# Performance work log

Hardware: AMD Instinct MI355X
Metric: run time of the kernel (lower is better)

Reference implementation:

```python
import jax, jax.numpy as jnp
import numpy as np

IN_FEATURES = 512
OUT_FEATURES = 512
BATCH = 1024


def setup_inputs() -> dict:
    key = jax.random.key(0)
    k_x, k_bw, k_ww, k_sc, k_tr, k_b = jax.random.split(key, 6)
    std = 1.0 / np.sqrt(IN_FEATURES)
    x = jax.random.normal(k_x, (BATCH, IN_FEATURES), dtype=jnp.float32)
    base_weight = jax.random.uniform(k_bw, (OUT_FEATURES, IN_FEATURES), jnp.float32, -std, std)
    wavelet_weights = jax.random.uniform(k_ww, (OUT_FEATURES, IN_FEATURES), jnp.float32, -std, std)
    # scale initialized to ones in the module; perturb slightly (kept positive) for a non-degenerate test
    scale = jnp.exp(0.1 * jax.random.normal(k_sc, (OUT_FEATURES, IN_FEATURES), dtype=jnp.float32))
    translation = 0.1 * jax.random.normal(k_tr, (OUT_FEATURES, IN_FEATURES), dtype=jnp.float32)
    bias = jax.random.uniform(k_b, (OUT_FEATURES,), jnp.float32, -std, std)
    return {"x": x, "base_weight": base_weight, "wavelet_weights": wavelet_weights,
            "scale": scale, "translation": translation, "bias": bias}


def reference(x, base_weight, wavelet_weights, scale, translation, bias):
    # base branch: SiLU then linear
    base_out = jnp.einsum("bi,oi->bo", jax.nn.silu(x), base_weight)
    # wavelet branch: broadcast x to (batch, out, in)
    xs = (x[:, None, :] - translation[None, :, :]) / scale[None, :, :]  # (B, O, I)
    wavelet = (xs * xs - 1.0) * jnp.exp(-0.5 * xs * xs)  # mexican hat
    wavelet_out = jnp.einsum("boi,oi->bo", wavelet, wavelet_weights)
    return base_out + wavelet_out + bias
```

## Files before the change

kernel.cpp:

```cpp
#include <hip/hip_runtime.h>


constexpr int IN_F  = 512;
constexpr int OUT_F = 512;
constexpr int BATCH = 1024;
constexpr int BT = 64, OT = 64;
constexpr int KS = 8;
constexpr int KR = IN_F / KS;
constexpr int IT = 16;
constexpr int PITCH = IT + 4;
constexpr int NCH = KR / IT;
constexpr int BO  = BATCH * OUT_F;

#define LOG2E 1.44269504088897f
#define C2f   (-0.72134752044448f)
#define NC2f  ( 0.72134752044448f)
#define RQf   (-0.84083003f)

typedef float v2f __attribute__((ext_vector_type(2)));

__device__ __forceinline__ float fexp2(float v) { return __builtin_amdgcn_exp2f(v); }
__device__ __forceinline__ float frcp(float v)  { return __builtin_amdgcn_rcpf(v); }
__device__ __forceinline__ v2f pkfma(v2f a, v2f b, v2f c) {
  return __builtin_elementwise_fma(a, b, c);
}
__device__ __forceinline__ float fsilu(float v) {
  return v * frcp(1.f + fexp2(v * -LOG2E));
}

__global__ __launch_bounds__(256, 4)
void wkan_main(const float* __restrict__ x, const float* __restrict__ basew,
               const float* __restrict__ wavew, const float* __restrict__ scale,
               const float* __restrict__ transl, const float* __restrict__ bias,
               float* __restrict__ partial, float* __restrict__ out, int use_ws)
{
  __shared__ float lx [BT * PITCH];
  __shared__ float lsx[BT * PITCH];
  __shared__ float la [OT * PITCH];
  __shared__ float lm [OT * PITCH];
  __shared__ float ln [OT * PITCH];
  __shared__ float lq [OT * PITCH];
  __shared__ float lb [OT * PITCH];

  const int tid = threadIdx.x;
  const int b0 = blockIdx.x * BT;
  const int o0 = blockIdx.y * OT;
  const int ks = blockIdx.z;
  const int k0 = ks * KR;

  const int srow = tid >> 2;
  const int sc4  = (tid & 3) * 4;
  const int lofs = srow * PITCH + sc4;

  const int to = tid & 15;
  const int tb = tid >> 4;

  v2f zz; zz.x = 0.f; zz.y = 0.f;
  v2f acc[4][4];
#pragma unroll
  for (int r = 0; r < 4; ++r)
#pragma unroll
    for (int c = 0; c < 4; ++c) acc[r][c] = zz;

  for (int kc = 0; kc < NCH; ++kc) {
    const int g = k0 + kc * IT + sc4;
    __syncthreads();
    {
      float4 xv = *(const float4*)(x + (size_t)(b0 + srow) * IN_F + g);
      float4 sx;
      sx.x = fsilu(xv.x); sx.y = fsilu(xv.y); sx.z = fsilu(xv.z); sx.w = fsilu(xv.w);
      *(float4*)(lx  + lofs) = xv;
      *(float4*)(lsx + lofs) = sx;

      float4 sv = *(const float4*)(scale  + (size_t)(o0 + srow) * IN_F + g);
      float4 tv = *(const float4*)(transl + (size_t)(o0 + srow) * IN_F + g);
      float4 av, mv, nv;
      {
        float a2, a2t;
        a2 = C2f * frcp(sv.x * sv.x); a2t = a2 * tv.x;
        av.x = a2; mv.x = -2.f * a2t; nv.x = fmaf(a2t, tv.x, NC2f);
        a2 = C2f * frcp(sv.y * sv.y); a2t = a2 * tv.y;
        av.y = a2; mv.y = -2.f * a2t; nv.y = fmaf(a2t, tv.y, NC2f);
        a2 = C2f * frcp(sv.z * sv.z); a2t = a2 * tv.z;
        av.z = a2; mv.z = -2.f * a2t; nv.z = fmaf(a2t, tv.z, NC2f);
        a2 = C2f * frcp(sv.w * sv.w); a2t = a2 * tv.w;
        av.w = a2; mv.w = -2.f * a2t; nv.w = fmaf(a2t, tv.w, NC2f);
      }
      *(float4*)(la + lofs) = av;
      *(float4*)(lm + lofs) = mv;
      *(float4*)(ln + lofs) = nv;

      float4 wv = *(const float4*)(wavew + (size_t)(o0 + srow) * IN_F + g);
      float4 qv;
      qv.x = wv.x * RQf; qv.y = wv.y * RQf; qv.z = wv.z * RQf; qv.w = wv.w * RQf;
      *(float4*)(lq + lofs) = qv;

      float4 bv = *(const float4*)(basew + (size_t)(o0 + srow) * IN_F + g);
      *(float4*)(lb + lofs) = bv;
    }
    __syncthreads();

    for (int ii = 0; ii < IT; ii += 4) {
      float4 xr[4], sr[4], x2[4];
#pragma unroll
      for (int r = 0; r < 4; ++r) {
        const int row = (tb + 16 * r) * PITCH + ii;
        xr[r] = *(const float4*)(lx + row);
        sr[r] = *(const float4*)(lsx + row);
        x2[r].x = xr[r].x * xr[r].x;
        x2[r].y = xr[r].y * xr[r].y;
        x2[r].z = xr[r].z * xr[r].z;
        x2[r].w = xr[r].w * xr[r].w;
      }
#pragma unroll
      for (int c = 0; c < 4; ++c) {
        const int orow = (to + 16 * c) * PITCH + ii;
        float4 A = *(const float4*)(la + orow);
        float4 M = *(const float4*)(lm + orow);
        float4 N = *(const float4*)(ln + orow);
        float4 Q = *(const float4*)(lq + orow);
        float4 B = *(const float4*)(lb + orow);
        v2f Al = {A.x, A.y}, Ah = {A.z, A.w};
        v2f Ml = {M.x, M.y}, Mh = {M.z, M.w};
        v2f Nl = {N.x, N.y}, Nh = {N.z, N.w};
        v2f Ql = {Q.x, Q.y}, Qh = {Q.z, Q.w};
        v2f Bl = {B.x, B.y}, Bh = {B.z, B.w};
#pragma unroll
        for (int r = 0; r < 4; ++r) {
          v2f xl  = {xr[r].x, xr[r].y}, xh  = {xr[r].z, xr[r].w};
          v2f x2l = {x2[r].x, x2[r].y}, x2h = {x2[r].z, x2[r].w};
          v2f sl  = {sr[r].x, sr[r].y}, sh  = {sr[r].z, sr[r].w};
          v2f p, e, gg;
          p = pkfma(Al, x2l, pkfma(Ml, xl, Nl));
          e.x = fexp2(p.x); e.y = fexp2(p.y);
          gg = p * Ql;
          acc[r][c] = pkfma(gg, e, acc[r][c]);
          acc[r][c] = pkfma(sl, Bl, acc[r][c]);
          p = pkfma(Ah, x2h, pkfma(Mh, xh, Nh));
          e.x = fexp2(p.x); e.y = fexp2(p.y);
          gg = p * Qh;
          acc[r][c] = pkfma(gg, e, acc[r][c]);
          acc[r][c] = pkfma(sh, Bh, acc[r][c]);
        }
      }
    }
  }

#pragma unroll
  for (int r = 0; r < 4; ++r) {
    const int br = b0 + tb + 16 * r;
#pragma unroll
    for (int c = 0; c < 4; ++c) {
      const int oc = o0 + to + 16 * c;
      float res = acc[r][c].x + acc[r][c].y;
      if (use_ws) {
        partial[(size_t)ks * BO + (size_t)br * OUT_F + oc] = res;
      } else {
        if (ks == 0) res += bias[oc];
        atomicAdd(out + (size_t)br * OUT_F + oc, res);
      }
    }
  }
}

__global__ __launch_bounds__(256)
void wkan_reduce(const float* __restrict__ partial, const float* __restrict__ bias,
                 float* __restrict__ out)
{
  const int i4 = (blockIdx.x * 256 + threadIdx.x) * 4;
  float4 r = *(const float4*)(bias + (i4 & (OUT_F - 1)));
#pragma unroll
  for (int k = 0; k < KS; ++k) {
    float4 a = *(const float4*)(partial + (size_t)k * BO + i4);
    r.x += a.x; r.y += a.y; r.z += a.z; r.w += a.w;
  }
  *(float4*)(out + i4) = r;
}

extern "C" void kernel_launch(void* const* d_in, const int* in_sizes, int n_in,
                              void* d_out, int out_size, void* d_ws, size_t ws_size,
                              hipStream_t stream) {
  const float* x  = (const float*)d_in[0];
  const float* bw = (const float*)d_in[1];
  const float* ww = (const float*)d_in[2];
  const float* sc = (const float*)d_in[3];
  const float* tr = (const float*)d_in[4];
  const float* bi = (const float*)d_in[5];
  float* out = (float*)d_out;

  const int use_ws = ws_size >= (size_t)KS * BO * sizeof(float) ? 1 : 0;
  if (!use_ws) {
    hipMemsetAsync(d_out, 0, (size_t)out_size * sizeof(float), stream);
  }
  dim3 grid(BATCH / BT, OUT_F / OT, KS);
  wkan_main<<<grid, dim3(256), 0, stream>>>(x, bw, ww, sc, tr, bi,
                                            (float*)d_ws, out, use_ws);
  if (use_ws) {
    wkan_reduce<<<dim3(BO / 1024), dim3(256), 0, stream>>>((const float*)d_ws, bi, out);
  }
}
```

Baseline: 115.2 us.

## Move SiLU base branch to fp16 MFMA and prefetch next chunk into registers

The SiLU-linear base branch leaves the scalar packed-FMA loop and runs as fp16 16x16x16 MFMA ops on half-precision tiles of silu(x) and base_weight. Its result goes through shared memory and is added to the wavelet accumulator at the end. The global loads for the next k-chunk are now issued before the compute of the current chunk to hide latency, and shared memory is merged into one aliased buffer. This removes VALU work from the exp-bound inner loop, but fp16 inputs lower accuracy and the extra LDS round trip adds syncs.

```diff
diff --git a/kernel.cpp b/kernel.cpp
--- a/kernel.cpp
+++ b/kernel.cpp
@@ -9,6 +9,8 @@
 constexpr int KR = IN_F / KS;
 constexpr int IT = 16;
 constexpr int PITCH = IT + 4;
+constexpr int HP = IT + 4;
+constexpr int LP = OT + 1;
 constexpr int NCH = KR / IT;
 constexpr int BO  = BATCH * OUT_F;
 
@@ -17,7 +19,9 @@
 #define NC2f  ( 0.72134752044448f)
 #define RQf   (-0.84083003f)
 
-typedef float v2f __attribute__((ext_vector_type(2)));
+typedef float v2f   __attribute__((ext_vector_type(2)));
+typedef float f32x4 __attribute__((ext_vector_type(4)));
+typedef _Float16 half4 __attribute__((ext_vector_type(4)));
 
 __device__ __forceinline__ float fexp2(float v) { return __builtin_amdgcn_exp2f(v); }
 __device__ __forceinline__ float frcp(float v)  { return __builtin_amdgcn_rcpf(v); }
@@ -27,6 +31,8 @@
 __device__ __forceinline__ float fsilu(float v) {
   return v * frcp(1.f + fexp2(v * -LOG2E));
 }
+
+constexpr int SMEM_F = 7680;
 
 __global__ __launch_bounds__(256, 4)
 void wkan_main(const float* __restrict__ x, const float* __restrict__ basew,
@@ -34,13 +40,15 @@
                const float* __restrict__ transl, const float* __restrict__ bias,
                float* __restrict__ partial, float* __restrict__ out, int use_ws)
 {
-  __shared__ float lx [BT * PITCH];
-  __shared__ float lsx[BT * PITCH];
-  __shared__ float la [OT * PITCH];
-  __shared__ float lm [OT * PITCH];
-  __shared__ float ln [OT * PITCH];
-  __shared__ float lq [OT * PITCH];
-  __shared__ float lb [OT * PITCH];
+  __shared__ float smem[SMEM_F];
+  float* lx = smem;
+  float* la = smem + 1280;
+  float* lm = smem + 2560;
+  float* ln = smem + 3840;
+  float* lq = smem + 5120;
+  _Float16* hx = (_Float16*)(smem + 6400);
+  _Float16* hb = (_Float16*)(smem + 7040);
+  float* lout = smem;
 
   const int tid = threadIdx.x;
   const int b0 = blockIdx.x * BT;
@@ -51,10 +59,16 @@
   const int srow = tid >> 2;
   const int sc4  = (tid & 3) * 4;
   const int lofs = srow * PITCH + sc4;
+  const int hofs = srow * HP + sc4;
 
   const int to = tid & 15;
   const int tb = tid >> 4;
 
+  const int lane = tid & 63;
+  const int wid  = tid >> 6;
+  const int frow = lane & 15;
+  const int kgrp = (lane >> 4) * 4;
+
   v2f zz; zz.x = 0.f; zz.y = 0.f;
   v2f acc[4][4];
 #pragma unroll
@@ -62,18 +76,31 @@
 #pragma unroll
     for (int c = 0; c < 4; ++c) acc[r][c] = zz;
 
+  f32x4 accb[4];
+#pragma unroll
+  for (int nt = 0; nt < 4; ++nt) accb[nt] = (f32x4)0.f;
+
+  float4 xv, sv, tv, wv, bv;
+  {
+    const int g = k0 + sc4;
+    xv = *(const float4*)(x      + (size_t)(b0 + srow) * IN_F + g);
+    sv = *(const float4*)(scale  + (size_t)(o0 + srow) * IN_F + g);
+    tv = *(const float4*)(transl + (size_t)(o0 + srow) * IN_F + g);
+    wv = *(const float4*)(wavew  + (size_t)(o0 + srow) * IN_F + g);
+    bv = *(const float4*)(basew  + (size_t)(o0 + srow) * IN_F + g);
+  }
+
   for (int kc = 0; kc < NCH; ++kc) {
-    const int g = k0 + kc * IT + sc4;
-    __syncthreads();
+    if (kc) __syncthreads();
     {
-      float4 xv = *(const float4*)(x + (size_t)(b0 + srow) * IN_F + g);
       float4 sx;
       sx.x = fsilu(xv.x); sx.y = fsilu(xv.y); sx.z = fsilu(xv.z); sx.w = fsilu(xv.w);
-      *(float4*)(lx  + lofs) = xv;
-      *(float4*)(lsx + lofs) = sx;
-
-      float4 sv = *(const float4*)(scale  + (size_t)(o0 + srow) * IN_F + g);
-      float4 tv = *(const float4*)(transl + (size_t)(o0 + srow) * IN_F + g);
+      *(float4*)(lx + lofs) = xv;
+      half4 h0;
+      h0[0] = (_Float16)sx.x; h0[1] = (_Float16)sx.y;
+      h0[2] = (_Float16)sx.z; h0[3] = (_Float16)sx.w;
+      *(half4*)(hx + hofs) = h0;
+
       float4 av, mv, nv;
       {
         float a2, a2t;
@@ -90,23 +117,41 @@
       *(float4*)(lm + lofs) = mv;
       *(float4*)(ln + lofs) = nv;
 
-      float4 wv = *(const float4*)(wavew + (size_t)(o0 + srow) * IN_F + g);
       float4 qv;
       qv.x = wv.x * RQf; qv.y = wv.y * RQf; qv.z = wv.z * RQf; qv.w = wv.w * RQf;
       *(float4*)(lq + lofs) = qv;
 
-      float4 bv = *(const float4*)(basew + (size_t)(o0 + srow) * IN_F + g);
-      *(float4*)(lb + lofs) = bv;
+      half4 hbv;
+      hbv[0] = (_Float16)bv.x; hbv[1] = (_Float16)bv.y;
+      hbv[2] = (_Float16)bv.z; hbv[3] = (_Float16)bv.w;
+      *(half4*)(hb + hofs) = hbv;
     }
     __syncthreads();
 
+    if (kc + 1 < NCH) {
+      const int g = k0 + (kc + 1) * IT + sc4;
+      xv = *(const float4*)(x      + (size_t)(b0 + srow) * IN_F + g);
+      sv = *(const float4*)(scale  + (size_t)(o0 + srow) * IN_F + g);
+      tv = *(const float4*)(transl + (size_t)(o0 + srow) * IN_F + g);
+      wv = *(const float4*)(wavew  + (size_t)(o0 + srow) * IN_F + g);
+      bv = *(const float4*)(basew  + (size_t)(o0 + srow) * IN_F + g);
+    }
+
+    {
+      half4 af = *(const half4*)(hx + (wid * 16 + frow) * HP + kgrp);
+#pragma unroll
+      for (int nt = 0; nt < 4; ++nt) {
+        half4 bf = *(const half4*)(hb + (nt * 16 + frow) * HP + kgrp);
+        accb[nt] = __builtin_amdgcn_mfma_f32_16x16x16f16(af, bf, accb[nt], 0, 0, 0);
+      }
+    }
+
     for (int ii = 0; ii < IT; ii += 4) {
-      float4 xr[4], sr[4], x2[4];
+      float4 xr[4], x2[4];
 #pragma unroll
       for (int r = 0; r < 4; ++r) {
         const int row = (tb + 16 * r) * PITCH + ii;
         xr[r] = *(const float4*)(lx + row);
-        sr[r] = *(const float4*)(lsx + row);
         x2[r].x = xr[r].x * xr[r].x;
         x2[r].y = xr[r].y * xr[r].y;
         x2[r].z = xr[r].z * xr[r].z;
@@ -119,32 +164,35 @@
         float4 M = *(const float4*)(lm + orow);
         float4 N = *(const float4*)(ln + orow);
         float4 Q = *(const float4*)(lq + orow);
-        float4 B = *(const float4*)(lb + orow);
         v2f Al = {A.x, A.y}, Ah = {A.z, A.w};
         v2f Ml = {M.x, M.y}, Mh = {M.z, M.w};
         v2f Nl = {N.x, N.y}, Nh = {N.z, N.w};
         v2f Ql = {Q.x, Q.y}, Qh = {Q.z, Q.w};
-        v2f Bl = {B.x, B.y}, Bh = {B.z, B.w};
 #pragma unroll
         for (int r = 0; r < 4; ++r) {
           v2f xl  = {xr[r].x, xr[r].y}, xh  = {xr[r].z, xr[r].w};
           v2f x2l = {x2[r].x, x2[r].y}, x2h = {x2[r].z, x2[r].w};
-          v2f sl  = {sr[r].x, sr[r].y}, sh  = {sr[r].z, sr[r].w};
           v2f p, e, gg;
           p = pkfma(Al, x2l, pkfma(Ml, xl, Nl));
           e.x = fexp2(p.x); e.y = fexp2(p.y);
           gg = p * Ql;
           acc[r][c] = pkfma(gg, e, acc[r][c]);
-          acc[r][c] = pkfma(sl, Bl, acc[r][c]);
           p = pkfma(Ah, x2h, pkfma(Mh, xh, Nh));
           e.x = fexp2(p.x); e.y = fexp2(p.y);
           gg = p * Qh;
           acc[r][c] = pkfma(gg, e, acc[r][c]);
-          acc[r][c] = pkfma(sh, Bh, acc[r][c]);
         }
       }
     }
   }
+
+  __syncthreads();
+#pragma unroll
+  for (int nt = 0; nt < 4; ++nt)
+#pragma unroll
+    for (int i = 0; i < 4; ++i)
+      lout[(wid * 16 + (lane >> 4) * 4 + i) * LP + nt * 16 + frow] = accb[nt][i];
+  __syncthreads();
 
 #pragma unroll
   for (int r = 0; r < 4; ++r) {
@@ -152,7 +200,8 @@
 #pragma unroll
     for (int c = 0; c < 4; ++c) {
       const int oc = o0 + to + 16 * c;
-      float res = acc[r][c].x + acc[r][c].y;
+      float res = acc[r][c].x + acc[r][c].y
+                + lout[(tb + 16 * r) * LP + to + 16 * c];
       if (use_ws) {
         partial[(size_t)ks * BO + (size_t)br * OUT_F + oc] = res;
       } else {
```

Result: slower. 126.5 us (+9.9%).
